# Performance work log

Measured on AMD Instinct MI355X. Metric: run time of the kernel, lower is better.

Reference implementation:

```python
import jax, jax.numpy as jnp
import numpy as np
import math

N, C, V, T = 64, 192, 25, 300
D = 192  # dim2

def setup_inputs() -> dict:
    key = jax.random.key(0)
    k0, k1, k2, k3 = jax.random.split(key, 4)
    x1 = jax.random.normal(k0, (N, C, V, T), dtype=jnp.float32)
    w1 = jax.random.normal(k1, (D, C), dtype=jnp.float32) * 0.05
    w2 = jax.random.normal(k2, (D, C), dtype=jnp.float32) * 0.05
    w_mask = jax.random.normal(k3, (1, C), dtype=jnp.float32) * 0.05
    return {"x1": x1, "w1": w1, "w2": w2, "w_mask": w_mask}

def reference(x1, w1, w2, w_mask):
    # 1x1 conv projections: contract over channel dim C -> D, layout [N,T,D,V]
    g1 = jnp.einsum('ncvt,dc->ntdv', x1, w1)
    g2 = jnp.einsum('ncvt,dc->ntdv', x1, w2)
    # mean-center over the joint axis V (matches g.mean(2) on [B, D, V])
    g1 = g1 - g1.mean(axis=-1, keepdims=True)
    g2 = g2 - g2.mean(axis=-1, keepdims=True)
    scale = math.sqrt(D)
    # sim_map[n,t,v,w] = sum_d g1[n,t,d,v] * g2[n,t,d,w]
    sim = jnp.einsum('ntdv,ntdw->ntvw', g1, g2) / scale
    # mask: 1x1 conv to 1 channel -> [N,T,V], broadcast over rows (added along last dim)
    mask = jnp.einsum('ncvt,c->ntv', x1, w_mask[0])  # [N,T,V]
    logits = sim + mask[:, :, None, :]
    out = jax.nn.softmax(logits, axis=-1)  # [N, T, V, V]
    return out
```

## Files before the change

### kernel.cpp

```cpp
#include <hip/hip_runtime.h>
#include <hip/hip_bf16.h>
#include <cstdint>
#include <cstddef>

#define NN 64
#define CC 192
#define VV 25
#define TTT 300
#define TC 16
#define NTC 19
#define GRID (NN*NTC)

#define MFRAG_OFF 40960
#define WML_OFF 77824

#define ROWT 88
#define TILE_B 35840
#define LDS_TOTAL (2*TILE_B)

typedef unsigned short u16;
typedef unsigned long long u64;
typedef short bf16x8 __attribute__((ext_vector_type(8)));
typedef float f32x4 __attribute__((ext_vector_type(4)));
typedef float f4 __attribute__((ext_vector_type(4)));

__device__ __forceinline__ u16 f2bf(float x) {
  union { float f; uint32_t u; } v; v.f = x;
  uint32_t r = v.u + 0x7fffu + ((v.u >> 16) & 1u);
  return (u16)(r >> 16);
}
__device__ __forceinline__ u64 pack4(f32x4 a) {
  return (u64)f2bf(a[0]) | ((u64)f2bf(a[1]) << 16) |
         ((u64)f2bf(a[2]) << 32) | ((u64)f2bf(a[3]) << 48);
}
__device__ __forceinline__ uint32_t pk2(float a, float b) {
  __hip_bfloat162 h = __float22bfloat162_rn(float2{a, b});
  uint32_t u; __builtin_memcpy(&u, &h, 4); return u;
}

__global__ __launch_bounds__(192) void prep(const float* __restrict__ w1,
                                            const float* __restrict__ w2,
                                            const float* __restrict__ wm,
                                            u16* __restrict__ mb) {
  int c2 = threadIdx.x, b = blockIdx.x;
  if (b < CC) {
    float s = 0.f;
    for (int d = 0; d < CC; ++d) s += w1[d * CC + b] * w2[d * CC + c2];
    u16 h = f2bf(s);
    int cc = b >> 5, half = (b >> 4) & 1, lr = b & 15;
    int ks = c2 >> 5, l8 = (c2 & 31) >> 3, e = c2 & 7;
    int lane = l8 * 16 + lr;
    mb[MFRAG_OFF + (((cc * 2 + half) * 6 + ks) * 64 + lane) * 8 + e] = h;
  } else {
    mb[WML_OFF + c2] = f2bf(wm[c2]);
  }
}

__device__ __forceinline__ void ldround(const float* __restrict__ xb, int ct,
                                        int tid, bool lastch, f4 pf[4]) {
  #pragma unroll
  for (int it = 0; it < 4; ++it) {
    int job = it * 1024 + tid;
    if (job < 3200) {
      int seg = job & 3;
      int r = job >> 2;
      int v = r >> 5, cl = r & 31;
      int sege = (lastch && seg == 3) ? 2 : seg;
      pf[it] = *(const f4*)(xb + (size_t)(ct * 32 + cl) * (VV * TTT) + v * TTT + sege * 4);
    }
  }
}

__global__ __launch_bounds__(1024, 4) void fused(const float* __restrict__ x1,
                                                 const u16* __restrict__ mb,
                                                 float* __restrict__ out) {
  __shared__ char lds[LDS_TOTAL];
  const int tid = threadIdx.x;
  const int wid = tid >> 6, lane = tid & 63, lr = lane & 15, lq = lane >> 4;
  char* YS = lds + wid * 3072;

  int b = blockIdx.x;
  int logical = (b & 7) * (GRID / 8) + (b >> 3);
  int n = logical / NTC;
  int ch = logical - n * NTC;
  int t0 = ch * TC;
  int t = t0 + wid;
  const bool lastch = (t0 + TC > TTT);

  const float* xb = x1 + (size_t)n * (CC * VV * TTT) + t0;

  bf16x8 sf[2][6];
  f4 pf[4];
  ldround(xb, 0, tid, lastch, pf);
  #pragma unroll
  for (int ct = 0; ct < 6; ++ct) {
    f4 cur[4];
    #pragma unroll
    for (int i = 0; i < 4; ++i) cur[i] = pf[i];
    if (ct < 5) ldround(xb, ct + 1, tid, lastch, pf);

    char* buf = lds + (ct & 1) * TILE_B;
    #pragma unroll
    for (int it = 0; it < 4; ++it) {
      int job = it * 1024 + tid;
      if (job < 3200) {
        int seg = job & 3;
        int r = job >> 2;
        int v = r >> 5, cl = r & 31;
        f4 a = cur[it];
        float p0 = __shfl_xor(a[0], 4);
        float p1 = __shfl_xor(a[1], 4);
        float p2 = __shfl_xor(a[2], 4);
        float p3 = __shfl_xor(a[3], 4);
        if (!(cl & 1)) {
          int colb = (cl >> 1) * 4;
          char* base = buf + (size_t)(seg * 4 * 25 + v) * ROWT + colb;
          *(uint32_t*)(base)             = pk2(a[0], p0);
          *(uint32_t*)(base + 25 * ROWT) = pk2(a[1], p1);
          *(uint32_t*)(base + 50 * ROWT) = pk2(a[2], p2);
          *(uint32_t*)(base + 75 * ROWT) = pk2(a[3], p3);
        }
      }
    }
    __syncthreads();
    #pragma unroll
    for (int j = 0; j < 2; ++j)
      sf[j][ct] = *(const bf16x8*)(buf + (wid * VV + j * 16 + lr) * ROWT + lq * 16);
  }
  __syncthreads();

  f32x4 pacc[2][2], macc[2];
  #pragma unroll
  for (int i = 0; i < 2; ++i) {
    macc[i] = (f32x4){0.f, 0.f, 0.f, 0.f};
    #pragma unroll
    for (int jx = 0; jx < 2; ++jx) pacc[i][jx] = (f32x4){0.f, 0.f, 0.f, 0.f};
  }

  const u16* mf = mb + MFRAG_OFF;
  #pragma unroll
  for (int cc = 0; cc < 6; ++cc) {
    f32x4 y00 = (f32x4){0.f,0.f,0.f,0.f}, y01 = y00, y10 = y00, y11 = y00;
    #pragma unroll
    for (int ks = 0; ks < 6; ++ks) {
      bf16x8 a0 = *(const bf16x8*)(mf + ((cc * 12 + ks) * 64 + lane) * 8);
      bf16x8 a1 = *(const bf16x8*)(mf + ((cc * 12 + 6 + ks) * 64 + lane) * 8);
      y00 = __builtin_amdgcn_mfma_f32_16x16x32_bf16(a0, sf[0][ks], y00, 0, 0, 0);
      y01 = __builtin_amdgcn_mfma_f32_16x16x32_bf16(a1, sf[0][ks], y01, 0, 0, 0);
      y10 = __builtin_amdgcn_mfma_f32_16x16x32_bf16(a0, sf[1][ks], y10, 0, 0, 0);
      y11 = __builtin_amdgcn_mfma_f32_16x16x32_bf16(a1, sf[1][ks], y11, 0, 0, 0);
    }
    *(u64*)(YS + (lr) * 80 + lq * 8) = pack4(y00);
    *(u64*)(YS + (lr) * 80 + 32 + lq * 8) = pack4(y01);
    *(u64*)(YS + (16 + lr) * 80 + lq * 8) = pack4(y10);
    *(u64*)(YS + (16 + lr) * 80 + 32 + lq * 8) = pack4(y11);

    bf16x8 wmf = *(const bf16x8*)(mb + WML_OFF + cc * 32 + lq * 8);
    #pragma unroll
    for (int vt = 0; vt < 2; ++vt) {
      bf16x8 A = sf[vt][cc];
      macc[vt] = __builtin_amdgcn_mfma_f32_16x16x32_bf16(A, wmf, macc[vt], 0, 0, 0);
      #pragma unroll
      for (int wt = 0; wt < 2; ++wt) {
        bf16x8 B = *(const bf16x8*)(YS + (wt * 16 + lr) * 80 + lq * 16);
        pacc[vt][wt] = __builtin_amdgcn_mfma_f32_16x16x32_bf16(A, B, pacc[vt][wt], 0, 0, 0);
      }
    }
  }

  float* SIMW = (float*)YS;
  #pragma unroll
  for (int vt = 0; vt < 2; ++vt)
    #pragma unroll
    for (int wt = 0; wt < 2; ++wt) {
      int w = wt * 16 + lr;
      if (w < VV) {
        #pragma unroll
        for (int i = 0; i < 4; ++i) {
          int v = vt * 16 + lq * 4 + i;
          if (v < VV) SIMW[v * 28 + w] = pacc[vt][wt][i];
        }
      }
    }
  if (lr == 0) {
    #pragma unroll
    for (int j = 0; j < 2; ++j)
      #pragma unroll
      for (int i = 0; i < 4; ++i) {
        int v = j * 16 + lq * 4 + i;
        if (v < VV) SIMW[26 * 28 + v] = macc[j][i];
      }
  }

  float rs = 0.f, cs = 0.f;
  if (lane < VV) {
    #pragma unroll
    for (int w = 0; w < VV; ++w) rs += SIMW[lane * 28 + w];
    #pragma unroll
    for (int v = 0; v < VV; ++v) cs += SIMW[v * 28 + lane];
    SIMW[25 * 28 + lane] = cs;
  }
  float x = (lane < VV) ? cs : 0.f;
  #pragma unroll
  for (int s = 1; s < 64; s <<= 1) x += __shfl_xor(x, s);
  const float tot = x;

  if (lane < VV) {
    const int v = lane;
    const float base = -rs * 0.04f + tot * 0.0016f;
    const float isc = 0.07216878364870323f;
    float l[VV];
    float mx = -1e30f;
    #pragma unroll
    for (int w = 0; w < VV; ++w) {
      float val = (SIMW[v * 28 + w] - SIMW[25 * 28 + w] * 0.04f + base) * isc +
                  SIMW[26 * 28 + w];
      l[w] = val;
      mx = fmaxf(mx, val);
    }
    float sum = 0.f;
    #pragma unroll
    for (int w = 0; w < VV; ++w) { float e = __expf(l[w] - mx); l[w] = e; sum += e; }
    float rsc = 1.0f / sum;
    #pragma unroll
    for (int w = 0; w < VV; ++w) SIMW[v * 28 + w] = l[w] * rsc;
  }

  if (t < TTT) {
    float* ob = out + (size_t)(n * TTT + t) * 625;
    for (int idx = lane; idx < 625; idx += 64) {
      int v = idx / VV, w = idx - v * VV;
      ob[idx] = SIMW[v * 28 + w];
    }
  }
}

extern "C" void kernel_launch(void* const* d_in, const int* in_sizes, int n_in,
                              void* d_out, int out_size, void* d_ws, size_t ws_size,
                              hipStream_t stream) {
  const float* x1 = (const float*)d_in[0];
  const float* w1 = (const float*)d_in[1];
  const float* w2 = (const float*)d_in[2];
  const float* wm = (const float*)d_in[3];
  float* out = (float*)d_out;
  u16* mb = (u16*)d_ws;

  hipLaunchKernelGGL(prep, dim3(CC + 1), dim3(CC), 0, stream, w1, w2, wm, mb);
  hipLaunchKernelGGL(fused, dim3(GRID), dim3(1024), 0, stream, x1, mb, out);
}
```

Baseline: 189.1 us.

## Simplify LDS staging stores, vectorize softmax LDS access, strength-reduce output indexing

Replaces the shuffle-and-pack bf16 staging (one half of lanes storing 32-bit pairs) with every lane storing its own 16-bit bf16 values directly, removing four cross-lane shuffles per job at the cost of more, narrower LDS stores. Unrolls the projection MFMA loop so each B fragment is loaded once explicitly. Vectorizes the softmax row reads and writes through LDS as float4 loads and stores, and replaces the divide/modulo index math in the output copy with incremental strength-reduced indexing. Together these aim to reduce instruction count in the staging and epilogue phases.

```diff
diff --git a/kernel.cpp b/kernel.cpp
--- a/kernel.cpp
+++ b/kernel.cpp
@@ -32,10 +32,6 @@
 __device__ __forceinline__ u64 pack4(f32x4 a) {
   return (u64)f2bf(a[0]) | ((u64)f2bf(a[1]) << 16) |
          ((u64)f2bf(a[2]) << 32) | ((u64)f2bf(a[3]) << 48);
-}
-__device__ __forceinline__ uint32_t pk2(float a, float b) {
-  __hip_bfloat162 h = __float22bfloat162_rn(float2{a, b});
-  uint32_t u; __builtin_memcpy(&u, &h, 4); return u;
 }
 
 __global__ __launch_bounds__(192) void prep(const float* __restrict__ w1,
@@ -108,18 +104,11 @@
         int r = job >> 2;
         int v = r >> 5, cl = r & 31;
         f4 a = cur[it];
-        float p0 = __shfl_xor(a[0], 4);
-        float p1 = __shfl_xor(a[1], 4);
-        float p2 = __shfl_xor(a[2], 4);
-        float p3 = __shfl_xor(a[3], 4);
-        if (!(cl & 1)) {
-          int colb = (cl >> 1) * 4;
-          char* base = buf + (size_t)(seg * 4 * 25 + v) * ROWT + colb;
-          *(uint32_t*)(base)             = pk2(a[0], p0);
-          *(uint32_t*)(base + 25 * ROWT) = pk2(a[1], p1);
-          *(uint32_t*)(base + 50 * ROWT) = pk2(a[2], p2);
-          *(uint32_t*)(base + 75 * ROWT) = pk2(a[3], p3);
-        }
+        char* base = buf + (size_t)(seg * 100 + v) * ROWT + cl * 2;
+        *(u16*)(base)             = f2bf(a[0]);
+        *(u16*)(base + 25 * ROWT) = f2bf(a[1]);
+        *(u16*)(base + 50 * ROWT) = f2bf(a[2]);
+        *(u16*)(base + 75 * ROWT) = f2bf(a[3]);
       }
     }
     __syncthreads();
@@ -156,16 +145,15 @@
     *(u64*)(YS + (16 + lr) * 80 + 32 + lq * 8) = pack4(y11);
 
     bf16x8 wmf = *(const bf16x8*)(mb + WML_OFF + cc * 32 + lq * 8);
-    #pragma unroll
-    for (int vt = 0; vt < 2; ++vt) {
-      bf16x8 A = sf[vt][cc];
-      macc[vt] = __builtin_amdgcn_mfma_f32_16x16x32_bf16(A, wmf, macc[vt], 0, 0, 0);
-      #pragma unroll
-      for (int wt = 0; wt < 2; ++wt) {
-        bf16x8 B = *(const bf16x8*)(YS + (wt * 16 + lr) * 80 + lq * 16);
-        pacc[vt][wt] = __builtin_amdgcn_mfma_f32_16x16x32_bf16(A, B, pacc[vt][wt], 0, 0, 0);
-      }
-    }
+    macc[0] = __builtin_amdgcn_mfma_f32_16x16x32_bf16(sf[0][cc], wmf, macc[0], 0, 0, 0);
+    macc[1] = __builtin_amdgcn_mfma_f32_16x16x32_bf16(sf[1][cc], wmf, macc[1], 0, 0, 0);
+
+    bf16x8 B0 = *(const bf16x8*)(YS + (lr) * 80 + lq * 16);
+    bf16x8 B1 = *(const bf16x8*)(YS + (16 + lr) * 80 + lq * 16);
+    pacc[0][0] = __builtin_amdgcn_mfma_f32_16x16x32_bf16(sf[0][cc], B0, pacc[0][0], 0, 0, 0);
+    pacc[0][1] = __builtin_amdgcn_mfma_f32_16x16x32_bf16(sf[0][cc], B1, pacc[0][1], 0, 0, 0);
+    pacc[1][0] = __builtin_amdgcn_mfma_f32_16x16x32_bf16(sf[1][cc], B0, pacc[1][0], 0, 0, 0);
+    pacc[1][1] = __builtin_amdgcn_mfma_f32_16x16x32_bf16(sf[1][cc], B1, pacc[1][1], 0, 0, 0);
   }
 
   float* SIMW = (float*)YS;
@@ -192,10 +180,15 @@
       }
   }
 
-  float rs = 0.f, cs = 0.f;
+  f32x4 r[6];
+  float r24 = 0.f, rs = 0.f, cs = 0.f;
   if (lane < VV) {
-    #pragma unroll
-    for (int w = 0; w < VV; ++w) rs += SIMW[lane * 28 + w];
+    const f32x4* rp = (const f32x4*)(SIMW + lane * 28);
+    #pragma unroll
+    for (int k = 0; k < 6; ++k) r[k] = rp[k];
+    r24 = SIMW[lane * 28 + 24];
+    f32x4 s4 = r[0] + r[1] + r[2] + r[3] + r[4] + r[5];
+    rs = s4[0] + s4[1] + s4[2] + s4[3] + r24;
     #pragma unroll
     for (int v = 0; v < VV; ++v) cs += SIMW[v * 28 + lane];
     SIMW[25 * 28 + lane] = cs;
@@ -209,28 +202,47 @@
     const int v = lane;
     const float base = -rs * 0.04f + tot * 0.0016f;
     const float isc = 0.07216878364870323f;
+    const f32x4* cp = (const f32x4*)(SIMW + 25 * 28);
+    const f32x4* mp = (const f32x4*)(SIMW + 26 * 28);
     float l[VV];
     float mx = -1e30f;
     #pragma unroll
-    for (int w = 0; w < VV; ++w) {
-      float val = (SIMW[v * 28 + w] - SIMW[25 * 28 + w] * 0.04f + base) * isc +
-                  SIMW[26 * 28 + w];
-      l[w] = val;
+    for (int k = 0; k < 6; ++k) {
+      f32x4 val = (r[k] - cp[k] * 0.04f + base) * isc + mp[k];
+      #pragma unroll
+      for (int j = 0; j < 4; ++j) {
+        l[k * 4 + j] = val[j];
+        mx = fmaxf(mx, val[j]);
+      }
+    }
+    {
+      float val = (r24 - SIMW[25 * 28 + 24] * 0.04f + base) * isc + SIMW[26 * 28 + 24];
+      l[24] = val;
       mx = fmaxf(mx, val);
     }
     float sum = 0.f;
     #pragma unroll
     for (int w = 0; w < VV; ++w) { float e = __expf(l[w] - mx); l[w] = e; sum += e; }
     float rsc = 1.0f / sum;
-    #pragma unroll
-    for (int w = 0; w < VV; ++w) SIMW[v * 28 + w] = l[w] * rsc;
+    f32x4* wp = (f32x4*)(SIMW + v * 28);
+    #pragma unroll
+    for (int k = 0; k < 6; ++k) {
+      f32x4 o = (f32x4){l[k*4] * rsc, l[k*4+1] * rsc, l[k*4+2] * rsc, l[k*4+3] * rsc};
+      wp[k] = o;
+    }
+    SIMW[v * 28 + 24] = l[24] * rsc;
   }
 
   if (t < TTT) {
     float* ob = out + (size_t)(n * TTT + t) * 625;
-    for (int idx = lane; idx < 625; idx += 64) {
-      int v = idx / VV, w = idx - v * VV;
-      ob[idx] = SIMW[v * 28 + w];
+    int v = (lane * 1311) >> 15;
+    int w = lane - v * 25;
+    #pragma unroll
+    for (int i = 0; i < 10; ++i) {
+      int idx = lane + i * 64;
+      if (idx < 625) ob[idx] = SIMW[v * 28 + w];
+      w += 14; v += 2;
+      if (w >= 25) { w -= 25; ++v; }
     }
   }
 }
```

Result: no change. 188.2 us (-0.5%).
